# Performance work log

Hardware: AMD Instinct MI355X
Metric: run time of the kernel (lower is better)

Reference implementation:

```python
import jax, jax.numpy as jnp
import numpy as np

B, H, D = 8, 2048, 2
K_COUPLE = 1.0
DT = 1.0
ALPHA_SCALE = 1.0


def setup_inputs() -> dict:
    key = jax.random.key(0)
    k1, k2, k3, k4, k5 = jax.random.split(key, 5)
    theta_prev = jax.random.normal(k1, (B, H, D), dtype=jnp.float32)
    gamma = jax.random.normal(k2, (B, H), dtype=jnp.float32)
    A = jax.random.uniform(k3, (B, H, H), dtype=jnp.float32)
    omega = jax.random.normal(k4, (H, D), dtype=jnp.float32) * 0.1
    kappa = jnp.ones((H, D), dtype=jnp.float32)
    direction_learner = jax.random.normal(k5, (H, H), dtype=jnp.float32) * 0.01
    return {"theta_prev": theta_prev, "gamma": gamma, "A": A,
            "omega": omega, "kappa": kappa, "direction_learner": direction_learner}


def reference(theta_prev, gamma, A, omega, kappa, direction_learner):
    b, h, d = theta_prev.shape
    # Symmetrized, positive lateral connectivity
    A_lat = 0.5 * (A + jnp.swapaxes(A, 1, 2))
    A_lat = jax.nn.relu(A_lat) + 1e-6  # [B,H,H]
    # OT surrogate: normalized cost, antisymmetric learned direction -> phase lag alpha
    cost = 1.0 / A_lat
    c_min = jnp.min(cost, axis=(1, 2), keepdims=True)
    c_max = jnp.max(cost, axis=(1, 2), keepdims=True)
    norm_cost = (cost - c_min) / (c_max - c_min + 1e-6)
    direction_mask = jnp.tanh(direction_learner - direction_learner.T)  # [H,H]
    alpha = (ALPHA_SCALE * direction_mask[None, :, :] * norm_cost)[..., None]  # [B,H,H,1]
    # Pairwise phase interaction: sum_j A_ij * sin(theta_j - theta_i - alpha_ij)
    theta_i = theta_prev[:, :, None, :]  # [B,H,1,D]
    theta_j = theta_prev[:, None, :, :]  # [B,1,H,D]
    phase_diff = theta_j - theta_i - alpha  # [B,H,H,D]
    interaction = jnp.sum(A_lat[..., None] * jnp.sin(phase_diff), axis=2)  # [B,H,D]
    coupling = (K_COUPLE / float(h)) * interaction
    drive = kappa * jnp.sin(gamma[..., None] - theta_prev)
    theta_dot = omega + coupling + drive
    return theta_prev + DT * theta_dot
```

## Files before the change

### kernel.cpp

```cpp
#include <hip/hip_runtime.h>
#include <hip/hip_fp16.h>

#define B 8
#define H 2048
#define D 2
#define HH (H*H)
#define TILE 64
#define NT (H/TILE)
#define NPAIR (NT*(NT+1)/2)
#define INV2PI 0.15915494309189535f
#define INVH (1.0f/2048.0f)

__device__ __forceinline__ float fsin(float x) { return __builtin_amdgcn_sinf(x * INV2PI); }
__device__ __forceinline__ float fcos(float x) { return __builtin_amdgcn_cosf(x * INV2PI); }

__device__ __forceinline__ void pair_decode(int tp, int& ti, int& tj) {
    ti = 0;
    while (tp >= NT - ti) { tp -= NT - ti; ti++; }
    tj = ti + tp;
}

__global__ __launch_bounds__(256) void k_pre(
    const float* __restrict__ A, const float* __restrict__ dl,
    const float* __restrict__ theta, const float* __restrict__ gamma,
    const float* __restrict__ omega, const float* __restrict__ kappa,
    float* __restrict__ out, float4* __restrict__ sc,
    __half* __restrict__ dmw,
    float* __restrict__ pmn, float* __restrict__ pmx) {
    int pair = blockIdx.x, b = blockIdx.y;
    int ti, tj; pair_decode(pair, ti, tj);
    int t = threadIdx.x, c = t & 63, r0 = t >> 6;

    __shared__ float l2[TILE][TILE + 1];
    const float* Ab = A + (size_t)b * HH;

    float v[16];
    #pragma unroll
    for (int k = 0; k < 16; k++)
        v[k] = Ab[(size_t)(tj * TILE + r0 + 4 * k) * H + ti * TILE + c];
    #pragma unroll
    for (int k = 0; k < 16; k++) l2[r0 + 4 * k][c] = v[k];
    __syncthreads();
    #pragma unroll
    for (int k = 0; k < 16; k++)
        v[k] = Ab[(size_t)(ti * TILE + r0 + 4 * k) * H + tj * TILE + c];

    float mn = 3.0e38f, mx = 0.f;
    #pragma unroll
    for (int k = 0; k < 16; k++) {
        int il = r0 + 4 * k;
        float al = fmaxf(0.5f * (v[k] + l2[c][il]), 0.f) + 1e-6f;
        mn = fminf(mn, al); mx = fmaxf(mx, al);
    }
    #pragma unroll
    for (int off = 32; off; off >>= 1) {
        mn = fminf(mn, __shfl_xor(mn, off));
        mx = fmaxf(mx, __shfl_xor(mx, off));
    }
    __shared__ float smn[4], smx[4];
    int wv = t >> 6, ln = t & 63;
    if (ln == 0) { smn[wv] = mn; smx[wv] = mx; }
    __syncthreads();
    if (t == 0) {
        for (int i = 1; i < 4; i++) { mn = fminf(mn, smn[i]); mx = fmaxf(mx, smx[i]); }
        pmn[b * NPAIR + pair] = mn;
        pmx[b * NPAIR + pair] = mx;
    }

    if (b == 0) {
        __syncthreads();
        float w2[16];
        #pragma unroll
        for (int k = 0; k < 16; k++)
            w2[k] = dl[(size_t)(tj * TILE + r0 + 4 * k) * H + ti * TILE + c];
        #pragma unroll
        for (int k = 0; k < 16; k++) l2[r0 + 4 * k][c] = w2[k];
        __syncthreads();
        #pragma unroll
        for (int k = 0; k < 16; k++)
            w2[k] = dl[(size_t)(ti * TILE + r0 + 4 * k) * H + tj * TILE + c];
        __half* dmp = dmw + (size_t)pair * (TILE * TILE);
        #pragma unroll
        for (int k = 0; k < 16; k++) {
            int il = r0 + 4 * k;
            float x = w2[k] - l2[c][il];
            float x2 = x * x;
            float dmv = x * fmaf(x2, fmaf(x2, 0.13333334f, -0.33333334f), 1.0f);
            dmp[il * TILE + c] = __float2half(dmv);
        }
    }

    if (b == 1 && pair < (B * H) / 256) {
        int g = pair * 256 + t;
        int i = g & (H - 1);
        float th0 = theta[(size_t)g * 2 + 0];
        float th1 = theta[(size_t)g * 2 + 1];
        sc[g] = make_float4(fsin(th0), fcos(th0), fsin(th1), fcos(th1));
        float gm = gamma[g];
        out[(size_t)g * 2 + 0] = th0 + omega[i * 2 + 0] + kappa[i * 2 + 0] * fsin(gm - th0);
        out[(size_t)g * 2 + 1] = th1 + omega[i * 2 + 1] + kappa[i * 2 + 1] * fsin(gm - th1);
    }
}

__global__ __launch_bounds__(256) void k_mmred(const float* __restrict__ pmn,
                                               const float* __restrict__ pmx,
                                               float* __restrict__ mmf) {
    int b = blockIdx.x, t = threadIdx.x;
    float mn = 3.0e38f, mx = 0.f;
    for (int k = t; k < NPAIR; k += 256) {
        mn = fminf(mn, pmn[b * NPAIR + k]);
        mx = fmaxf(mx, pmx[b * NPAIR + k]);
    }
    #pragma unroll
    for (int off = 32; off; off >>= 1) {
        mn = fminf(mn, __shfl_xor(mn, off));
        mx = fmaxf(mx, __shfl_xor(mx, off));
    }
    __shared__ float smn[4], smx[4];
    int wv = t >> 6, ln = t & 63;
    if (ln == 0) { smn[wv] = mn; smx[wv] = mx; }
    __syncthreads();
    if (t == 0) {
        for (int i = 1; i < 4; i++) { mn = fminf(mn, smn[i]); mx = fmaxf(mx, smx[i]); }
        mmf[b * 2 + 0] = mn;
        mmf[b * 2 + 1] = mx;
    }
}

__global__ __launch_bounds__(256) void k_main(
    const float* __restrict__ A, const __half* __restrict__ dmw,
    const float4* __restrict__ sc, const float* __restrict__ mmf,
    float* __restrict__ out) {
    int pair = blockIdx.x, b = blockIdx.y;
    int ti, tj; pair_decode(pair, ti, tj);
    bool diag = (ti == tj);
    int t = threadIdx.x, w = t >> 6, ln = t & 63;
    int c = ln, r0 = t >> 6;

    __shared__ float l2[TILE][TILE + 1];
    __shared__ float4 ldssc[TILE];
    __shared__ float red[4][TILE][2];

    float amin = mmf[b * 2 + 0];
    float amax = mmf[b * 2 + 1];
    float cmin = 1.0f / amax, cmax = 1.0f / amin;
    float invr = 1.0f / (cmax - cmin + 1e-6f);
    float ncb = cmin * invr;

    const float* Ab = A + (size_t)b * HH;
    const float4* scb = sc + (size_t)b * H;

    float v[16];
    #pragma unroll
    for (int k = 0; k < 16; k++)
        v[k] = Ab[(size_t)(tj * TILE + r0 + 4 * k) * H + ti * TILE + c];
    #pragma unroll
    for (int k = 0; k < 16; k++) l2[r0 + 4 * k][c] = v[k];

    if (t < TILE) ldssc[t] = scb[ti * TILE + t];

    int j = tj * TILE + ln;
    float4 scj = scb[j];
    float sj0 = scj.x, cj0 = scj.y, sj1 = scj.z, cj1 = scj.w;
    __syncthreads();

    const __half* dmp = dmw + (size_t)pair * (TILE * TILE);

    float accj0 = 0.f, accj1 = 0.f;
    float rs = 0.f;

    #pragma unroll
    for (int k = 0; k < 16; k++) {
        int il = w * 16 + k;
        float4 sciv = ldssc[il];
        float si0 = sciv.x, ci0 = sciv.y, si1 = sciv.z, ci1 = sciv.w;

        float aij = Ab[(size_t)(ti * TILE + il) * H + tj * TILE + ln];
        float aji = l2[ln][il];
        float al = fmaxf(0.5f * (aij + aji), 0.f) + 1e-6f;
        float dmv = __half2float(dmp[il * TILE + ln]);
        float cost = __builtin_amdgcn_rcpf(al);
        float nc = fmaf(cost, invr, -ncb);
        float alpha = dmv * nc;
        float a2 = alpha * alpha;
        float sa = alpha * fmaf(a2, -0.16666667f, 1.0f);
        float ca = fmaf(a2, -0.5f, 1.0f);
        float sd0 = fmaf(sj0, ci0, -cj0 * si0);
        float cd0 = fmaf(cj0, ci0,  sj0 * si0);
        float c0 = al * fmaf(sd0, ca, -cd0 * sa);
        float sd1 = fmaf(sj1, ci1, -cj1 * si1);
        float cd1 = fmaf(cj1, ci1,  sj1 * si1);
        float c1 = al * fmaf(sd1, ca, -cd1 * sa);

        accj0 -= c0;
        accj1 -= c1;

        float s0 = c0, s1 = c1;
        #pragma unroll
        for (int off = 32; off; off >>= 1) {
            s0 += __shfl_xor(s0, off);
            s1 += __shfl_xor(s1, off);
        }
        if (ln == 2 * k)     rs = s0;
        if (ln == 2 * k + 1) rs = s1;
    }

    if (ln < 32) {
        int k = ln >> 1, d = ln & 1;
        int i = ti * TILE + w * 16 + k;
        atomicAdd(&out[(size_t)(b * H + i) * 2 + d], rs * INVH);
    }

    red[w][ln][0] = accj0; red[w][ln][1] = accj1;
    __syncthreads();
    if (!diag && t < 128) {
        int jl = t >> 1, d = t & 1;
        float cs = red[0][jl][d] + red[1][jl][d] + red[2][jl][d] + red[3][jl][d];
        atomicAdd(&out[(size_t)(b * H + tj * TILE + jl) * 2 + d], cs * INVH);
    }
}


__global__ void k_init_fb(unsigned int* mm) {
    int t = threadIdx.x;
    if (t < B * 2) mm[t] = (t & 1) ? 0u : 0x7f800000u;
}

__global__ __launch_bounds__(256) void k_minmax_fb(const float* __restrict__ A,
                                                   unsigned int* __restrict__ mm) {
    int b = blockIdx.y;
    int tp = blockIdx.x;
    int ti, tj; pair_decode(tp, ti, tj);

    __shared__ float l2[TILE][TILE + 1];
    const float* Ab = A + (size_t)b * HH;
    int t = threadIdx.x;
    int c = t & 63, r0 = t >> 6;

    #pragma unroll
    for (int k = 0; k < 16; k++)
        l2[r0 + 4 * k][c] = Ab[(size_t)(tj * TILE + r0 + 4 * k) * H + ti * TILE + c];
    __syncthreads();

    float mn = 3.0e38f, mx = 0.f;
    #pragma unroll
    for (int k = 0; k < 16; k++) {
        int il = r0 + 4 * k;
        float aij = Ab[(size_t)(ti * TILE + il) * H + tj * TILE + c];
        float v = fmaxf(0.5f * (aij + l2[c][il]), 0.f) + 1e-6f;
        mn = fminf(mn, v); mx = fmaxf(mx, v);
    }
    #pragma unroll
    for (int off = 32; off; off >>= 1) {
        mn = fminf(mn, __shfl_xor(mn, off));
        mx = fmaxf(mx, __shfl_xor(mx, off));
    }
    __shared__ float smn[4], smx[4];
    int wv = t >> 6, ln = t & 63;
    if (ln == 0) { smn[wv] = mn; smx[wv] = mx; }
    __syncthreads();
    if (t == 0) {
        for (int i = 1; i < 4; i++) { mn = fminf(mn, smn[i]); mx = fmaxf(mx, smx[i]); }
        atomicMin(&mm[b * 2 + 0], __float_as_uint(mn));
        atomicMax(&mm[b * 2 + 1], __float_as_uint(mx));
    }
}

__global__ __launch_bounds__(1024) void k_main_fb(
    const float* __restrict__ theta, const float* __restrict__ gamma,
    const float* __restrict__ A, const float* __restrict__ omega,
    const float* __restrict__ kappa, const float* __restrict__ dl,
    const unsigned int* __restrict__ mm, float* __restrict__ out) {
    int b = blockIdx.y;
    int i0 = blockIdx.x * TILE;
    int t = threadIdx.x;
    int w = t >> 6, ln = t & 63;

    __shared__ float aT[TILE][TILE + 1];
    __shared__ float dT[TILE][TILE + 1];
    __shared__ float thI[4][TILE];
    __shared__ float thJ[4][TILE];

    float amin = __uint_as_float(mm[b * 2 + 0]);
    float amax = __uint_as_float(mm[b * 2 + 1]);
    float cmin = 1.0f / amax, cmax = 1.0f / amin;
    float invr = 1.0f / (cmax - cmin + 1e-6f);

    if (t < 128) {
        int il = t & 63, d = t >> 6;
        float th = theta[(size_t)(b * H + i0 + il) * D + d];
        thI[d * 2 + 0][il] = fsin(th);
        thI[d * 2 + 1][il] = fcos(th);
    }
    __syncthreads();

    float si[4][2], ci[4][2];
    #pragma unroll
    for (int k = 0; k < 4; k++)
        #pragma unroll
        for (int d = 0; d < 2; d++) {
            si[k][d] = thI[d * 2 + 0][w * 4 + k];
            ci[k][d] = thI[d * 2 + 1][w * 4 + k];
        }

    float acc[4][2] = {};
    const float* Ab = A + (size_t)b * HH;

    for (int jt = 0; jt < NT; jt++) {
        int j0 = jt * TILE;
        __syncthreads();
        #pragma unroll
        for (int k = 0; k < 4; k++) {
            int r = w * 4 + k;
            aT[r][ln] = Ab[(size_t)(j0 + r) * H + i0 + ln];
            dT[r][ln] = dl[(size_t)(j0 + r) * H + i0 + ln];
        }
        if (t < 128) {
            int jl = t & 63, d = t >> 6;
            float th = theta[(size_t)(b * H + j0 + jl) * D + d];
            thJ[d * 2 + 0][jl] = fsin(th);
            thJ[d * 2 + 1][jl] = fcos(th);
        }
        __syncthreads();

        float sj0 = thJ[0][ln], cj0 = thJ[1][ln];
        float sj1 = thJ[2][ln], cj1 = thJ[3][ln];
        const float* arow = Ab + (size_t)(i0 + w * 4) * H + j0 + ln;
        const float* drow = dl + (size_t)(i0 + w * 4) * H + j0 + ln;
        #pragma unroll
        for (int k = 0; k < 4; k++) {
            float aij = arow[(size_t)k * H];
            float dij = drow[(size_t)k * H];
            float aji = aT[ln][w * 4 + k];
            float dji = dT[ln][w * 4 + k];
            float al = fmaxf(0.5f * (aij + aji), 0.f) + 1e-6f;
            float cost = __builtin_amdgcn_rcpf(al);
            float nc = (cost - cmin) * invr;
            float x = dij - dji;
            float x2 = x * x;
            float dmv = x * fmaf(x2, fmaf(x2, 0.13333334f, -0.33333334f), 1.0f);
            float alpha = dmv * nc;
            float sa = fsin(alpha), ca = fcos(alpha);
            {
                float sd = sj0 * ci[k][0] - cj0 * si[k][0];
                float cd = cj0 * ci[k][0] + sj0 * si[k][0];
                acc[k][0] = fmaf(al, sd * ca - cd * sa, acc[k][0]);
            }
            {
                float sd = sj1 * ci[k][1] - cj1 * si[k][1];
                float cd = cj1 * ci[k][1] + sj1 * si[k][1];
                acc[k][1] = fmaf(al, sd * ca - cd * sa, acc[k][1]);
            }
        }
    }

    #pragma unroll
    for (int k = 0; k < 4; k++)
        #pragma unroll
        for (int d = 0; d < 2; d++)
            #pragma unroll
            for (int off = 32; off; off >>= 1)
                acc[k][d] += __shfl_xor(acc[k][d], off);

    if (ln < 8) {
        int k = ln >> 1, d = ln & 1;
        int i = i0 + w * 4 + k;
        size_t idx = (size_t)(b * H + i) * D + d;
        float chosen = __shfl(acc[k][d], k * 2 + d);
        float th = theta[idx];
        float drv = kappa[i * D + d] * fsin(gamma[b * H + i] - th);
        out[idx] = th + (omega[i * D + d] + (1.0f / H) * chosen + drv);
    }
}


extern "C" void kernel_launch(void* const* d_in, const int* in_sizes, int n_in,
                              void* d_out, int out_size, void* d_ws, size_t ws_size,
                              hipStream_t stream) {
    const float* theta = (const float*)d_in[0];
    const float* gamma = (const float*)d_in[1];
    const float* A     = (const float*)d_in[2];
    const float* omega = (const float*)d_in[3];
    const float* kappa = (const float*)d_in[4];
    const float* dl    = (const float*)d_in[5];
    float* out = (float*)d_out;

    float* mmf = (float*)d_ws;
    float* pmn = (float*)((char*)d_ws + 1024);
    float* pmx = pmn + B * NPAIR;
    float4* sc = (float4*)((char*)d_ws + 65536);
    __half* dmw = (__half*)((char*)d_ws + 65536 + 262144);
    size_t need = 65536 + 262144 + (size_t)NPAIR * TILE * TILE * 2;

    if (ws_size >= need) {
        hipLaunchKernelGGL(k_pre, dim3(NPAIR, B), dim3(256), 0, stream,
                           A, dl, theta, gamma, omega, kappa, out, sc, dmw, pmn, pmx);
        hipLaunchKernelGGL(k_mmred, dim3(B), dim3(256), 0, stream, pmn, pmx, mmf);
        hipLaunchKernelGGL(k_main, dim3(NPAIR, B), dim3(256), 0, stream,
                           A, dmw, sc, mmf, out);
    } else {
        unsigned int* mm = (unsigned int*)d_ws;
        hipLaunchKernelGGL(k_init_fb, dim3(1), dim3(64), 0, stream, mm);
        hipLaunchKernelGGL(k_minmax_fb, dim3(NPAIR, B), dim3(256), 0, stream, A, mm);
        hipLaunchKernelGGL(k_main_fb, dim3(NT, B), dim3(1024), 0, stream,
                           theta, gamma, A, omega, kappa, dl, mm, out);
    }
}
```

Before: 263.1 us.

## Replace symmetric pair-tile main kernel with full-row sweep and factored sin sums

The main kernel no longer exploits A's symmetry with paired tiles and per-row shuffle reductions. Each block now sweeps a row tile over a chunk of columns. It factors sin(θj−θi−α) into per-i sin/cos products of accumulated sums, so the inner loop only does FMAs. The direction mask is stored as a full H×H half matrix (both signs) and the min/max reduction is folded into k_main, which drops one launch. In exchange A is read roughly twice instead of once, and there are more uncoalesced column reads (A[j*H+i]) and a larger workspace.

```diff
diff --git a/kernel.cpp b/kernel.cpp
--- a/kernel.cpp
+++ b/kernel.cpp
@@ -8,6 +8,9 @@
 #define TILE 64
 #define NT (H/TILE)
 #define NPAIR (NT*(NT+1)/2)
+#define NJC 8
+#define JC (H/NJC)
+#define SUB 16
 #define INV2PI 0.15915494309189535f
 #define INVH (1.0f/2048.0f)
 
@@ -79,14 +82,23 @@
         #pragma unroll
         for (int k = 0; k < 16; k++)
             w2[k] = dl[(size_t)(ti * TILE + r0 + 4 * k) * H + tj * TILE + c];
-        __half* dmp = dmw + (size_t)pair * (TILE * TILE);
+        float dmv[16];
         #pragma unroll
         for (int k = 0; k < 16; k++) {
             int il = r0 + 4 * k;
             float x = w2[k] - l2[c][il];
             float x2 = x * x;
-            float dmv = x * fmaf(x2, fmaf(x2, 0.13333334f, -0.33333334f), 1.0f);
-            dmp[il * TILE + c] = __float2half(dmv);
+            dmv[k] = x * fmaf(x2, fmaf(x2, 0.13333334f, -0.33333334f), 1.0f);
+            dmw[(size_t)(ti * TILE + il) * H + tj * TILE + c] = __float2half(dmv[k]);
+        }
+        __syncthreads();
+        #pragma unroll
+        for (int k = 0; k < 16; k++) l2[c][r0 + 4 * k] = dmv[k];
+        __syncthreads();
+        #pragma unroll
+        for (int k = 0; k < 16; k++) {
+            int rr = r0 + 4 * k;
+            dmw[(size_t)(tj * TILE + rr) * H + ti * TILE + c] = __float2half(-l2[rr][c]);
         }
     }
 
@@ -102,121 +114,94 @@
     }
 }
 
-__global__ __launch_bounds__(256) void k_mmred(const float* __restrict__ pmn,
-                                               const float* __restrict__ pmx,
-                                               float* __restrict__ mmf) {
-    int b = blockIdx.x, t = threadIdx.x;
-    float mn = 3.0e38f, mx = 0.f;
-    for (int k = t; k < NPAIR; k += 256) {
-        mn = fminf(mn, pmn[b * NPAIR + k]);
-        mx = fmaxf(mx, pmx[b * NPAIR + k]);
-    }
-    #pragma unroll
-    for (int off = 32; off; off >>= 1) {
-        mn = fminf(mn, __shfl_xor(mn, off));
-        mx = fmaxf(mx, __shfl_xor(mx, off));
-    }
-    __shared__ float smn[4], smx[4];
-    int wv = t >> 6, ln = t & 63;
-    if (ln == 0) { smn[wv] = mn; smx[wv] = mx; }
-    __syncthreads();
-    if (t == 0) {
-        for (int i = 1; i < 4; i++) { mn = fminf(mn, smn[i]); mx = fmaxf(mx, smx[i]); }
-        mmf[b * 2 + 0] = mn;
-        mmf[b * 2 + 1] = mx;
-    }
-}
-
-__global__ __launch_bounds__(256) void k_main(
+__global__ __launch_bounds__(256, 8) void k_main(
     const float* __restrict__ A, const __half* __restrict__ dmw,
-    const float4* __restrict__ sc, const float* __restrict__ mmf,
+    const float4* __restrict__ sc,
+    const float* __restrict__ pmn, const float* __restrict__ pmx,
     float* __restrict__ out) {
-    int pair = blockIdx.x, b = blockIdx.y;
-    int ti, tj; pair_decode(pair, ti, tj);
-    bool diag = (ti == tj);
+    int it = blockIdx.x, jc = blockIdx.y, b = blockIdx.z;
     int t = threadIdx.x, w = t >> 6, ln = t & 63;
-    int c = ln, r0 = t >> 6;
-
-    __shared__ float l2[TILE][TILE + 1];
-    __shared__ float4 ldssc[TILE];
+    int i0 = it * TILE;
+    int i = i0 + ln;
+
+    __shared__ float tile[4][SUB][TILE + 1];
     __shared__ float red[4][TILE][2];
-
-    float amin = mmf[b * 2 + 0];
-    float amax = mmf[b * 2 + 1];
+    __shared__ float smm[2];
+
+    if (t < 64) {
+        float mn = 3.0e38f, mx = 0.f;
+        for (int k = t; k < NPAIR; k += 64) {
+            mn = fminf(mn, pmn[b * NPAIR + k]);
+            mx = fmaxf(mx, pmx[b * NPAIR + k]);
+        }
+        #pragma unroll
+        for (int off = 32; off; off >>= 1) {
+            mn = fminf(mn, __shfl_xor(mn, off));
+            mx = fmaxf(mx, __shfl_xor(mx, off));
+        }
+        if (t == 0) { smm[0] = mn; smm[1] = mx; }
+    }
+
+    const float* Ab = A + (size_t)b * HH;
+    const float4* scb = sc + (size_t)b * H;
+    float4 sci = scb[i];
+    float si0 = sci.x, ci0 = sci.y, si1 = sci.z, ci1 = sci.w;
+    __syncthreads();
+
+    float amin = smm[0], amax = smm[1];
     float cmin = 1.0f / amax, cmax = 1.0f / amin;
     float invr = 1.0f / (cmax - cmin + 1e-6f);
     float ncb = cmin * invr;
 
-    const float* Ab = A + (size_t)b * HH;
-    const float4* scb = sc + (size_t)b * H;
-
-    float v[16];
-    #pragma unroll
-    for (int k = 0; k < 16; k++)
-        v[k] = Ab[(size_t)(tj * TILE + r0 + 4 * k) * H + ti * TILE + c];
-    #pragma unroll
-    for (int k = 0; k < 16; k++) l2[r0 + 4 * k][c] = v[k];
-
-    if (t < TILE) ldssc[t] = scb[ti * TILE + t];
-
-    int j = tj * TILE + ln;
-    float4 scj = scb[j];
-    float sj0 = scj.x, cj0 = scj.y, sj1 = scj.z, cj1 = scj.w;
-    __syncthreads();
-
-    const __half* dmp = dmw + (size_t)pair * (TILE * TILE);
-
-    float accj0 = 0.f, accj1 = 0.f;
-    float rs = 0.f;
-
-    #pragma unroll
-    for (int k = 0; k < 16; k++) {
-        int il = w * 16 + k;
-        float4 sciv = ldssc[il];
-        float si0 = sciv.x, ci0 = sciv.y, si1 = sciv.z, ci1 = sciv.w;
-
-        float aij = Ab[(size_t)(ti * TILE + il) * H + tj * TILE + ln];
-        float aji = l2[ln][il];
-        float al = fmaxf(0.5f * (aij + aji), 0.f) + 1e-6f;
-        float dmv = __half2float(dmp[il * TILE + ln]);
-        float cost = __builtin_amdgcn_rcpf(al);
-        float nc = fmaf(cost, invr, -ncb);
-        float alpha = dmv * nc;
-        float a2 = alpha * alpha;
-        float sa = alpha * fmaf(a2, -0.16666667f, 1.0f);
-        float ca = fmaf(a2, -0.5f, 1.0f);
-        float sd0 = fmaf(sj0, ci0, -cj0 * si0);
-        float cd0 = fmaf(cj0, ci0,  sj0 * si0);
-        float c0 = al * fmaf(sd0, ca, -cd0 * sa);
-        float sd1 = fmaf(sj1, ci1, -cj1 * si1);
-        float cd1 = fmaf(cj1, ci1,  sj1 * si1);
-        float c1 = al * fmaf(sd1, ca, -cd1 * sa);
-
-        accj0 -= c0;
-        accj1 -= c1;
-
-        float s0 = c0, s1 = c1;
-        #pragma unroll
-        for (int off = 32; off; off >>= 1) {
-            s0 += __shfl_xor(s0, off);
-            s1 += __shfl_xor(s1, off);
-        }
-        if (ln == 2 * k)     rs = s0;
-        if (ln == 2 * k + 1) rs = s1;
-    }
-
-    if (ln < 32) {
-        int k = ln >> 1, d = ln & 1;
-        int i = ti * TILE + w * 16 + k;
-        atomicAdd(&out[(size_t)(b * H + i) * 2 + d], rs * INVH);
-    }
-
-    red[w][ln][0] = accj0; red[w][ln][1] = accj1;
-    __syncthreads();
-    if (!diag && t < 128) {
-        int jl = t >> 1, d = t & 1;
-        float cs = red[0][jl][d] + red[1][jl][d] + red[2][jl][d] + red[3][jl][d];
-        atomicAdd(&out[(size_t)(b * H + tj * TILE + jl) * 2 + d], cs * INVH);
+    float a1s0 = 0.f, a1c0 = 0.f, a1s1 = 0.f, a1c1 = 0.f;
+    float a2s0 = 0.f, a2c0 = 0.f, a2s1 = 0.f, a2c1 = 0.f;
+
+    int jbase = jc * JC + w * (JC / 4);
+    int rr = ln >> 2, cc = (ln & 3) * 4;
+    for (int st = 0; st < JC / 4 / SUB; st++) {
+        int j0 = jbase + st * SUB;
+        #pragma unroll
+        for (int g = 0; g < 4; g++) {
+            int r = rr + g * 16;
+            float4 v = *(const float4*)(Ab + (size_t)(i0 + r) * H + j0 + cc);
+            tile[w][cc + 0][r] = v.x;
+            tile[w][cc + 1][r] = v.y;
+            tile[w][cc + 2][r] = v.z;
+            tile[w][cc + 3][r] = v.w;
+        }
+        #pragma unroll
+        for (int jj = 0; jj < SUB; jj++) {
+            int j = j0 + jj;
+            float4 scj = scb[j];
+            float aji = Ab[(size_t)j * H + i];
+            float dmT = __half2float(dmw[(size_t)j * H + i]);
+            float aij = tile[w][jj][ln];
+            float al = fmaxf(0.5f * (aij + aji), 0.f) + 1e-6f;
+            float qp  = dmT * fmaf(-ncb, al, invr);
+            float rcp = __builtin_amdgcn_rcpf(al);
+            float ap  = qp * rcp;
+            float m1  = fmaf(-0.5f, qp * ap, al);
+            float m2p = fmaf(-0.16666667f * ap * ap, qp, qp);
+            a1s0 = fmaf(m1, scj.x, a1s0);
+            a1c0 = fmaf(m1, scj.y, a1c0);
+            a1s1 = fmaf(m1, scj.z, a1s1);
+            a1c1 = fmaf(m1, scj.w, a1c1);
+            a2s0 = fmaf(m2p, scj.x, a2s0);
+            a2c0 = fmaf(m2p, scj.y, a2c0);
+            a2s1 = fmaf(m2p, scj.z, a2s1);
+            a2c1 = fmaf(m2p, scj.w, a2c1);
+        }
+    }
+
+    float p0 = ci0 * (a1s0 + a2c0) - si0 * (a1c0 - a2s0);
+    float p1 = ci1 * (a1s1 + a2c1) - si1 * (a1c1 - a2s1);
+
+    red[w][ln][0] = p0; red[w][ln][1] = p1;
+    __syncthreads();
+    if (t < 128) {
+        int il = t >> 1, d = t & 1;
+        float s = red[0][il][d] + red[1][il][d] + red[2][il][d] + red[3][il][d];
+        atomicAdd(&out[(size_t)(b * H + i0 + il) * 2 + d], s * INVH);
     }
 }
 
@@ -385,19 +370,17 @@
     const float* dl    = (const float*)d_in[5];
     float* out = (float*)d_out;
 
-    float* mmf = (float*)d_ws;
     float* pmn = (float*)((char*)d_ws + 1024);
     float* pmx = pmn + B * NPAIR;
     float4* sc = (float4*)((char*)d_ws + 65536);
     __half* dmw = (__half*)((char*)d_ws + 65536 + 262144);
-    size_t need = 65536 + 262144 + (size_t)NPAIR * TILE * TILE * 2;
+    size_t need = 65536 + 262144 + (size_t)HH * 2;
 
     if (ws_size >= need) {
         hipLaunchKernelGGL(k_pre, dim3(NPAIR, B), dim3(256), 0, stream,
                            A, dl, theta, gamma, omega, kappa, out, sc, dmw, pmn, pmx);
-        hipLaunchKernelGGL(k_mmred, dim3(B), dim3(256), 0, stream, pmn, pmx, mmf);
-        hipLaunchKernelGGL(k_main, dim3(NPAIR, B), dim3(256), 0, stream,
-                           A, dmw, sc, mmf, out);
+        hipLaunchKernelGGL(k_main, dim3(NT, NJC, B), dim3(256), 0, stream,
+                           A, dmw, sc, pmn, pmx, out);
     } else {
         unsigned int* mm = (unsigned int*)d_ws;
         hipLaunchKernelGGL(k_init_fb, dim3(1), dim3(64), 0, stream, mm);
```

Result: slower. 274.9 us (+4.5%).
